# Kernel tuning notes

Hardware: AMD Instinct MI355X
Metric: run time of the kernel (lower is better)

Reference implementation:

```python
import jax, jax.numpy as jnp
import numpy as np

EMBED_DIM = 1024
NUM_HEADS = 16
HEAD_DIM = EMBED_DIM // NUM_HEADS


def setup_inputs() -> dict:
    key = jax.random.key(0)
    ks = jax.random.split(key, 11)
    B, S, D = 2, 2048, EMBED_DIM
    s = 1.0 / np.sqrt(D)
    inp = {
        "q": jax.random.normal(ks[0], (B, S, D), jnp.float32),
        "k": jax.random.normal(ks[1], (B, S, D), jnp.float32),
        "v": jax.random.normal(ks[2], (B, S, D), jnp.float32),
        # Linear params stored as (in, out) so y = x @ W + b
        "wq": jax.random.uniform(ks[3], (D, D), jnp.float32, -s, s),
        "bq": jax.random.uniform(ks[4], (D,), jnp.float32, -s, s),
        "wk": jax.random.uniform(ks[5], (D, D), jnp.float32, -s, s),
        "bk": jax.random.uniform(ks[6], (D,), jnp.float32, -s, s),
        "wv": jax.random.uniform(ks[7], (D, D), jnp.float32, -s, s),
        "bv": jax.random.uniform(ks[8], (D,), jnp.float32, -s, s),
        "wo": jax.random.uniform(ks[9], (D, D), jnp.float32, -s, s),
        "bo": jax.random.uniform(ks[10], (D,), jnp.float32, -s, s),
    }
    return inp


def reference(q, k, v, wq, bq, wk, bk, wv, bv, wo, bo):
    B, S, D = q.shape
    H, Hd = NUM_HEADS, HEAD_DIM
    temperature = Hd ** 0.5

    def proj(x, w, b):
        # (B, S, D) -> (B, H, S, Hd)
        y = x @ w + b
        return y.reshape(B, S, H, Hd).transpose(0, 2, 1, 3)

    qh = proj(q, wq, bq)
    kh = proj(k, wk, bk)
    vh = proj(v, wv, bv)

    # naive attention with materialized [B, H, S, S] scores (faithful to source)
    scores = jnp.einsum("bhqd,bhkd->bhqk", qh / temperature, kh)
    attn = jax.nn.softmax(scores, axis=-1)
    ctx = jnp.einsum("bhqk,bhkd->bhqd", attn, vh)

    ctx = ctx.transpose(0, 2, 1, 3).reshape(B, S, D)
    out = ctx @ wo + bo
    return out, attn
```

## Files before the change

### kernel.cpp

```cpp
#include <hip/hip_runtime.h>

#define S_   2048
#define D_   1024

typedef __attribute__((ext_vector_type(8))) __bf16 bf16x8;
typedef __attribute__((ext_vector_type(4))) __bf16 bf16x4;
typedef __attribute__((ext_vector_type(4))) float f32x4;
typedef __attribute__((ext_vector_type(4))) float float4v;
typedef __attribute__((ext_vector_type(2))) unsigned int u32x2;
typedef __attribute__((ext_vector_type(4))) unsigned int u32x4;

#define XQ_OFF   0
#define XK_OFF   4194304
#define XV_OFF   8388608
#define WQT_OFF  12582912
#define WKT_OFF  13631488
#define WVT_OFF  14680064
#define WOT_OFF  15728640
#define QH_OFF   16777216
#define KH_OFF   20971520
#define VHT_OFF  25165824
#define CTX_OFF  29360128
#define WS_BYTES 67108864ULL

#if __has_builtin(__builtin_amdgcn_exp2f)
#define EXP2(x) __builtin_amdgcn_exp2f(x)
#else
#define EXP2(x) __expf((x) * 0.69314718056f)
#endif
#define QSCALE 0.1803368801f

__device__ __forceinline__ unsigned short f2b(float f) {
  unsigned u = __builtin_bit_cast(unsigned, f);
  u += 0x7fffu + ((u >> 16) & 1u);
  return (unsigned short)(u >> 16);
}
__device__ __forceinline__ float b2f(unsigned s) {
  return __builtin_bit_cast(float, s << 16);
}

__global__ __launch_bounds__(256) void cvt_all(const float* __restrict__ q,
    const float* __restrict__ k, const float* __restrict__ v,
    const float* __restrict__ wq, const float* __restrict__ wk,
    const float* __restrict__ wv, const float* __restrict__ wo,
    short* __restrict__ ws) {
  __shared__ float tile[32][33];
  int b = blockIdx.x, tid = threadIdx.x;
  if (b < 12288) {
    int y = b >> 12, x = b & 4095;
    const float* src = (y == 0) ? q : (y == 1) ? k : v;
    short* dst = ws + (size_t)y * 4194304;
    size_t t = (size_t)x * 256 + tid;
    float4v f = *(const float4v*)(src + t * 4);
    u32x2 p;
    p[0] = (unsigned)f2b(f[0]) | ((unsigned)f2b(f[1]) << 16);
    p[1] = (unsigned)f2b(f[2]) | ((unsigned)f2b(f[3]) << 16);
    *(u32x2*)(dst + t * 4) = p;
    return;
  }
  int b2 = b - 12288;
  int z = b2 >> 10, rem = b2 & 1023;
  int by = rem >> 5, bx = rem & 31;
  const float* W = (z == 0) ? wq : (z == 1) ? wk : (z == 2) ? wv : wo;
  short* Wt = ws + WQT_OFF + (size_t)z * 1048576;
  int tx = tid & 31, ty = tid >> 5;
#pragma unroll
  for (int i = 0; i < 4; ++i)
    tile[ty + i * 8][tx] =
        W[(size_t)(by * 32 + ty + i * 8) * D_ + bx * 32 + tx];
  __syncthreads();
#pragma unroll
  for (int i = 0; i < 4; ++i)
    Wt[(size_t)(bx * 32 + ty + i * 8) * D_ + by * 32 + tx] =
        (short)f2b(tile[tx][ty + i * 8]);
}

__device__ __forceinline__ void stage_tile(const short* __restrict__ g,
                                           short* l, int w, int lane) {
  int lrow = lane >> 3, lcol = (lane & 7) * 8;
#pragma unroll
  for (int c = 0; c < 4; ++c) {
    int seg = c * 4 + w;
    const short* gp = g + (size_t)(seg * 8 + lrow) * 1024 + lcol;
    short* lp = l + seg * 512 + lane * 8;
    __builtin_amdgcn_global_load_lds(
        (const __attribute__((address_space(1))) void*)gp,
        (__attribute__((address_space(3))) void*)lp, 16, 0, 0);
  }
}

__global__ __launch_bounds__(256) void gemm_bf16(short* __restrict__ ws,
    const float* __restrict__ bq, const float* __restrict__ bk,
    const float* __restrict__ bv, const float* __restrict__ bo,
    float* __restrict__ out, int mode_base) {
  const int tid = threadIdx.x, lane = tid & 63, w = tid >> 6;
  const int wm = w >> 1, wn = w & 1;
  const int ln15 = lane & 15, g = lane >> 4;
  const int bm = blockIdx.y, bn = blockIdx.x;
  const int mode = (mode_base == 3) ? 3 : (int)blockIdx.z;

  const short* A; const short* Bt; const float* bias;
  if (mode == 0)      { A = ws + XQ_OFF;  Bt = ws + WQT_OFF; bias = bq; }
  else if (mode == 1) { A = ws + XK_OFF;  Bt = ws + WKT_OFF; bias = bk; }
  else if (mode == 2) { A = ws + XV_OFF;  Bt = ws + WVT_OFF; bias = bv; }
  else                { A = ws + CTX_OFF; Bt = ws + WOT_OFF; bias = bo; }

  __shared__ short smem[2][2][8192];
  short (*sA)[8192] = smem[0];
  short (*sB)[8192] = smem[1];

  f32x4 acc[4][4] = {};

  const short* Ab = A + (size_t)bm * 128 * 1024;
  const short* Bb = Bt + (size_t)bn * 128 * 1024;

  stage_tile(Ab, sA[0], w, lane);
  stage_tile(Bb, sB[0], w, lane);
  __syncthreads();

  int cur = 0;
#pragma unroll 1
  for (int kt = 0; kt < 16; ++kt) {
    if (kt < 15) {
      stage_tile(Ab + (kt + 1) * 64, sA[cur ^ 1], w, lane);
      stage_tile(Bb + (kt + 1) * 64, sB[cur ^ 1], w, lane);
    }
#pragma unroll
    for (int kk = 0; kk < 2; ++kk) {
      bf16x8 af[4], bfr[4];
#pragma unroll
      for (int m = 0; m < 4; ++m)
        af[m] = *(const bf16x8*)&sA[cur][(wm * 64 + m * 16 + ln15) * 64 + kk * 32 + g * 8];
#pragma unroll
      for (int n = 0; n < 4; ++n)
        bfr[n] = *(const bf16x8*)&sB[cur][(wn * 64 + n * 16 + ln15) * 64 + kk * 32 + g * 8];
#pragma unroll
      for (int m = 0; m < 4; ++m)
#pragma unroll
        for (int n = 0; n < 4; ++n)
          acc[m][n] = __builtin_amdgcn_mfma_f32_16x16x32_bf16(af[m], bfr[n], acc[m][n], 0, 0, 0);
    }
    __syncthreads();
    cur ^= 1;
  }

  float bb[4];
#pragma unroll
  for (int n = 0; n < 4; ++n) bb[n] = bias[bn * 128 + wn * 64 + n * 16 + ln15];

  if (mode == 3) {
#pragma unroll
    for (int m = 0; m < 4; ++m) {
      int row0 = bm * 128 + wm * 64 + m * 16 + g * 4;
#pragma unroll
      for (int n = 0; n < 4; ++n) {
        int col = bn * 128 + wn * 64 + n * 16 + ln15;
#pragma unroll
        for (int r = 0; r < 4; ++r)
          out[(size_t)(row0 + r) * 1024 + col] = acc[m][n][r] + bb[n];
      }
    }
    return;
  }

  float sc = (mode == 0) ? QSCALE : 1.0f;
  short (*tile)[136] = (short(*)[136])smem;
#pragma unroll
  for (int m = 0; m < 4; ++m)
#pragma unroll
    for (int n = 0; n < 4; ++n)
#pragma unroll
      for (int r = 0; r < 4; ++r)
        tile[wm * 64 + m * 16 + g * 4 + r][wn * 64 + n * 16 + ln15] =
            (short)f2b((acc[m][n][r] + bb[n]) * sc);
  __syncthreads();

  if (mode == 2) {
    int dcol = tid >> 1, sh = (tid & 1) * 64;
    int colg = bn * 128 + dcol, h = colg >> 6, hd = colg & 63;
    int b = bm >> 4, sblk = bm & 15;
    short* dst = ws + VHT_OFF +
                 ((size_t)((b * 16 + h) * 16 + sblk)) * 8192 + hd * 128 + sh;
#pragma unroll
    for (int j = 0; j < 8; ++j) {
      u32x4 pk;
#pragma unroll
      for (int q = 0; q < 4; ++q) {
        unsigned lo = (unsigned short)tile[sh + j * 8 + q * 2][dcol];
        unsigned hi = (unsigned short)tile[sh + j * 8 + q * 2 + 1][dcol];
        pk[q] = lo | (hi << 16);
      }
      *(u32x4*)(dst + j * 8) = pk;
    }
  } else {
    int r = tid >> 1, sh = (tid & 1) * 64;
    int colg = bn * 128 + sh, h = colg >> 6;
    int sg = bm * 128 + r, b = sg >> 11, sl = sg & 2047;
    short* dst = ws + ((mode == 0) ? QH_OFF : KH_OFF) +
                 (((size_t)(b * 16 + h)) * 2048 + sl) * 64;
#pragma unroll
    for (int j = 0; j < 8; ++j)
      *(u32x4*)(dst + j * 8) = *(const u32x4*)&tile[r][sh + j * 8];
  }
}

__global__ __launch_bounds__(512) void attn_k(short* __restrict__ ws,
                                              float* __restrict__ attn) {
  const int tid = threadIdx.x, lane = tid & 63, w = tid >> 6;
  const int ln15 = lane & 15, g = lane >> 4, ln7 = lane & 7;
  int bid = blockIdx.x;
  int qt = (bid >> 3) & 15;
  int bh = (bid & 7) + 8 * (bid >> 7);
  const int q0 = qt * 128;

  const short* Q  = ws + QH_OFF  + ((size_t)bh * 2048 + q0) * 64;
  const short* K  = ws + KH_OFF  + (size_t)bh * 2048 * 64;
  const short* Vt = ws + VHT_OFF + (size_t)bh * 131072;

  __shared__ short sKV[4][4096];
  __shared__ short PlA[128][72];
  __shared__ short PlB[128][72];

  const int srow = tid >> 3, sc = tid & 7;
  const int scsw = sc ^ (srow & 7);
  const int sdst = tid * 8;

#define STAGE1(t1, b)                                                         \
  do {                                                                        \
    __builtin_amdgcn_global_load_lds(                                         \
        (const __attribute__((address_space(1))) void*)(K + ((t1) * 128 + srow) * 64 + scsw * 8),      \
        (__attribute__((address_space(3))) void*)(&sKV[2 * (b)][sdst]), 16, 0, 0);                     \
    __builtin_amdgcn_global_load_lds(                                         \
        (const __attribute__((address_space(1))) void*)(K + ((t1) * 128 + 64 + srow) * 64 + scsw * 8), \
        (__attribute__((address_space(3))) void*)(&sKV[2 * (b) + 1][sdst]), 16, 0, 0);                 \
  } while (0)
#define STAGE_K2(kt)                                                          \
  __builtin_amdgcn_global_load_lds(                                           \
      (const __attribute__((address_space(1))) void*)(K + ((kt) * 64 + srow) * 64 + scsw * 8),         \
      (__attribute__((address_space(3))) void*)(&sKV[(kt) & 1][sdst]), 16, 0, 0)
#define STAGE_V2(kt)                                                          \
  __builtin_amdgcn_global_load_lds(                                           \
      (const __attribute__((address_space(1))) void*)(Vt + ((kt) >> 1) * 8192 + srow * 128 + ((kt) & 1) * 64 + scsw * 8), \
      (__attribute__((address_space(3))) void*)(&sKV[2 + ((kt) & 1)][sdst]), 16, 0, 0)

  bf16x8 qf0 = *(const bf16x8*)&Q[(w * 16 + ln15) * 64 + g * 8];
  bf16x8 qf1 = *(const bf16x8*)&Q[(w * 16 + ln15) * 64 + 32 + g * 8];

  STAGE1(0, 0);
  asm volatile("s_waitcnt vmcnt(0)" ::: "memory");
  __builtin_amdgcn_s_barrier();

  float ps0 = 0.f, ps1 = 0.f;
#pragma unroll 1
  for (int t = 0; t < 16; ++t) {
    int b = t & 1;
    if (t < 15) STAGE1(t + 1, b ^ 1);
#pragma unroll
    for (int m = 0; m < 8; ++m) {
      const short* kbase = &sKV[2 * b + (m >> 2)][((m * 16 + ln15) & 63) * 64];
      bf16x8 ka0 = *(const bf16x8*)&kbase[(g ^ ln7) * 8];
      bf16x8 ka1 = *(const bf16x8*)&kbase[((4 + g) ^ ln7) * 8];
      f32x4 c = {0.f, 0.f, 0.f, 0.f};
      c = __builtin_amdgcn_mfma_f32_16x16x32_bf16(ka0, qf0, c, 0, 0, 0);
      c = __builtin_amdgcn_mfma_f32_16x16x32_bf16(ka1, qf1, c, 0, 0, 0);
      ps0 += EXP2(c[0]) + EXP2(c[1]);
      ps1 += EXP2(c[2]) + EXP2(c[3]);
    }
    asm volatile("s_waitcnt vmcnt(0)" ::: "memory");
    __builtin_amdgcn_s_barrier();
  }
  float ps = ps0 + ps1;
  ps += __shfl_xor(ps, 16, 64);
  ps += __shfl_xor(ps, 32, 64);
  float ri = 1.0f / ps;

#define QKT_BODY(kti, PLW)                                                    \
  do {                                                                        \
    _Pragma("unroll") for (int m = 0; m < 4; ++m) {                           \
      const short* kbase = &sKV[(kti) & 1][(m * 16 + ln15) * 64];             \
      bf16x8 ka0 = *(const bf16x8*)&kbase[(g ^ ln7) * 8];                     \
      bf16x8 ka1 = *(const bf16x8*)&kbase[((4 + g) ^ ln7) * 8];               \
      f32x4 c = {0.f, 0.f, 0.f, 0.f};                                         \
      c = __builtin_amdgcn_mfma_f32_16x16x32_bf16(ka0, qf0, c, 0, 0, 0);      \
      c = __builtin_amdgcn_mfma_f32_16x16x32_bf16(ka1, qf1, c, 0, 0, 0);      \
      bf16x4 pb;                                                              \
      pb[0] = (__bf16)(EXP2(c[0]) * ri);                                      \
      pb[1] = (__bf16)(EXP2(c[1]) * ri);                                      \
      pb[2] = (__bf16)(EXP2(c[2]) * ri);                                      \
      pb[3] = (__bf16)(EXP2(c[3]) * ri);                                      \
      *(bf16x4*)&PLW[w * 16 + ln15][m * 16 + g * 4] = pb;                     \
    }                                                                         \
  } while (0)

#define FULL_BODY(i, PLR, PLW)                                                \
  do {                                                                        \
    if ((i) < 30) STAGE_K2((i) + 2);                                          \
    if ((i) < 31) STAGE_V2((i) + 1);                                          \
    if ((i) < 31) QKT_BODY((i) + 1, PLW);                                     \
    _Pragma("unroll") for (int kk = 0; kk < 2; ++kk) {                        \
      bf16x8 pa = *(const bf16x8*)&PLR[w * 16 + ln15][kk * 32 + g * 8];       \
      _Pragma("unroll") for (int n = 0; n < 4; ++n) {                         \
        const short* vbase = &sKV[2 + ((i) & 1)][(n * 16 + ln15) * 64];       \
        bf16x8 vb = *(const bf16x8*)&vbase[((kk * 4 + g) ^ ln7) * 8];         \
        cacc[n] = __builtin_amdgcn_mfma_f32_16x16x32_bf16(pa, vb, cacc[n], 0, 0, 0); \
      }                                                                       \
    }                                                                         \
    {                                                                         \
      float* ab = attn + ((size_t)(bh * 2048 + q0 + w * 16)) * 2048 + (i) * 64 + lane; \
      _Pragma("unroll") for (int r = 0; r < 16; ++r)                          \
        ab[(size_t)r * 2048] = b2f((unsigned short)PLR[w * 16 + r][lane]);    \
    }                                                                         \
    asm volatile("s_waitcnt vmcnt(16)" ::: "memory");                         \
    __builtin_amdgcn_s_barrier();                                             \
  } while (0)

  f32x4 cacc[4] = {};

  STAGE_K2(0);
  STAGE_V2(0);
  STAGE_K2(1);
  asm volatile("s_waitcnt vmcnt(0)" ::: "memory");
  __builtin_amdgcn_s_barrier();
  QKT_BODY(0, PlA);
  asm volatile("s_waitcnt lgkmcnt(0)" ::: "memory");
  __builtin_amdgcn_s_barrier();

#pragma unroll 1
  for (int i2 = 0; i2 < 32; i2 += 2) {
    FULL_BODY(i2, PlA, PlB);
    FULL_BODY(i2 + 1, PlB, PlA);
  }

  {
    short* Pw = &PlA[w * 16][0];
#pragma unroll
    for (int n = 0; n < 4; ++n)
#pragma unroll
      for (int r = 0; r < 4; ++r)
        Pw[(g * 4 + r) * 72 + n * 16 + ln15] = (short)f2b(cacc[n][r]);
    asm volatile("s_waitcnt lgkmcnt(0)" ::: "memory");
    __builtin_amdgcn_sched_barrier(0);
    int b = bh >> 4, h = bh & 15;
    int row = lane >> 3, col = (lane & 7) * 8;
#pragma unroll
    for (int i = 0; i < 2; ++i) {
      int q = q0 + w * 16 + i * 8 + row;
      u32x4 pk = *(const u32x4*)&Pw[(i * 8 + row) * 72 + col];
      *(u32x4*)&ws[CTX_OFF + ((size_t)(b * 2048 + q)) * 1024 + h * 64 + col] = pk;
    }
  }
#undef STAGE1
#undef STAGE_K2
#undef STAGE_V2
#undef QKT_BODY
#undef FULL_BODY
}

extern "C" void kernel_launch(void* const* d_in, const int* in_sizes, int n_in,
                              void* d_out, int out_size, void* d_ws, size_t ws_size,
                              hipStream_t stream) {
  const float* q  = (const float*)d_in[0];
  const float* k  = (const float*)d_in[1];
  const float* v  = (const float*)d_in[2];
  const float* wq = (const float*)d_in[3];
  const float* bq = (const float*)d_in[4];
  const float* wk = (const float*)d_in[5];
  const float* bk = (const float*)d_in[6];
  const float* wv = (const float*)d_in[7];
  const float* bv = (const float*)d_in[8];
  const float* wo = (const float*)d_in[9];
  const float* bo = (const float*)d_in[10];
  float* out  = (float*)d_out;
  float* attn = out + 4194304;
  short* ws = (short*)d_ws;
  if (ws_size < WS_BYTES) return;

  cvt_all<<<dim3(16384), 256, 0, stream>>>(q, k, v, wq, wk, wv, wo, ws);
  gemm_bf16<<<dim3(8, 32, 3), 256, 0, stream>>>(ws, bq, bk, bv, bo, out, 0);
  attn_k<<<dim3(512), 512, 0, stream>>>(ws, attn);
  gemm_bf16<<<dim3(8, 32, 1), 256, 0, stream>>>(ws, bq, bk, bv, bo, out, 3);
}
```

Measured before the change: 271.8 us.

## Triple-buffer K/V staging and batch attn stores into 256-column float4 writes

Restructures the attention main loop so K and V tiles use a three-deep LDS ring prefetched two steps ahead. QK^T and PV for the same tile now run back-to-back inside one iteration, replacing the previous skewed ping-pong P buffers. Probabilities for four key tiles accumulate in a wider LDS buffer and are written to the attn output as float4 stores every 256 columns, instead of scalar stores per 64 columns. This aims to improve global store efficiency and load latency hiding. The cost is more LDS, which may reduce occupancy, and an added lgkmcnt wait between QK and PV within each step.

```diff
diff --git a/kernel.cpp b/kernel.cpp
--- a/kernel.cpp
+++ b/kernel.cpp
@@ -217,31 +217,30 @@
   const short* K  = ws + KH_OFF  + (size_t)bh * 2048 * 64;
   const short* Vt = ws + VHT_OFF + (size_t)bh * 131072;
 
-  __shared__ short sKV[4][4096];
-  __shared__ short PlA[128][72];
-  __shared__ short PlB[128][72];
+  __shared__ short sStage[6][4096];
+  __shared__ short Pbig[128][264];
 
   const int srow = tid >> 3, sc = tid & 7;
   const int scsw = sc ^ (srow & 7);
   const int sdst = tid * 8;
 
+#define STAGE_K2(kt)                                                          \
+  __builtin_amdgcn_global_load_lds(                                           \
+      (const __attribute__((address_space(1))) void*)(K + ((kt) * 64 + srow) * 64 + scsw * 8),         \
+      (__attribute__((address_space(3))) void*)(&sStage[(kt) % 3][sdst]), 16, 0, 0)
+#define STAGE_V2(kt)                                                          \
+  __builtin_amdgcn_global_load_lds(                                           \
+      (const __attribute__((address_space(1))) void*)(Vt + ((kt) >> 1) * 8192 + srow * 128 + ((kt) & 1) * 64 + scsw * 8), \
+      (__attribute__((address_space(3))) void*)(&sStage[3 + (kt) % 3][sdst]), 16, 0, 0)
 #define STAGE1(t1, b)                                                         \
   do {                                                                        \
     __builtin_amdgcn_global_load_lds(                                         \
         (const __attribute__((address_space(1))) void*)(K + ((t1) * 128 + srow) * 64 + scsw * 8),      \
-        (__attribute__((address_space(3))) void*)(&sKV[2 * (b)][sdst]), 16, 0, 0);                     \
+        (__attribute__((address_space(3))) void*)(&sStage[(b)][sdst]), 16, 0, 0);                      \
     __builtin_amdgcn_global_load_lds(                                         \
         (const __attribute__((address_space(1))) void*)(K + ((t1) * 128 + 64 + srow) * 64 + scsw * 8), \
-        (__attribute__((address_space(3))) void*)(&sKV[2 * (b) + 1][sdst]), 16, 0, 0);                 \
+        (__attribute__((address_space(3))) void*)(&sStage[3 + (b)][sdst]), 16, 0, 0);                  \
   } while (0)
-#define STAGE_K2(kt)                                                          \
-  __builtin_amdgcn_global_load_lds(                                           \
-      (const __attribute__((address_space(1))) void*)(K + ((kt) * 64 + srow) * 64 + scsw * 8),         \
-      (__attribute__((address_space(3))) void*)(&sKV[(kt) & 1][sdst]), 16, 0, 0)
-#define STAGE_V2(kt)                                                          \
-  __builtin_amdgcn_global_load_lds(                                           \
-      (const __attribute__((address_space(1))) void*)(Vt + ((kt) >> 1) * 8192 + srow * 128 + ((kt) & 1) * 64 + scsw * 8), \
-      (__attribute__((address_space(3))) void*)(&sKV[2 + ((kt) & 1)][sdst]), 16, 0, 0)
 
   bf16x8 qf0 = *(const bf16x8*)&Q[(w * 16 + ln15) * 64 + g * 8];
   bf16x8 qf1 = *(const bf16x8*)&Q[(w * 16 + ln15) * 64 + 32 + g * 8];
@@ -257,7 +256,8 @@
     if (t < 15) STAGE1(t + 1, b ^ 1);
 #pragma unroll
     for (int m = 0; m < 8; ++m) {
-      const short* kbase = &sKV[2 * b + (m >> 2)][((m * 16 + ln15) & 63) * 64];
+      const short* kbase =
+          &sStage[(m >> 2) * 3 + b][((m * 16 + ln15) & 63) * 64];
       bf16x8 ka0 = *(const bf16x8*)&kbase[(g ^ ln7) * 8];
       bf16x8 ka1 = *(const bf16x8*)&kbase[((4 + g) ^ ln7) * 8];
       f32x4 c = {0.f, 0.f, 0.f, 0.f};
@@ -274,70 +274,87 @@
   ps += __shfl_xor(ps, 32, 64);
   float ri = 1.0f / ps;
 
-#define QKT_BODY(kti, PLW)                                                    \
-  do {                                                                        \
-    _Pragma("unroll") for (int m = 0; m < 4; ++m) {                           \
-      const short* kbase = &sKV[(kti) & 1][(m * 16 + ln15) * 64];             \
-      bf16x8 ka0 = *(const bf16x8*)&kbase[(g ^ ln7) * 8];                     \
-      bf16x8 ka1 = *(const bf16x8*)&kbase[((4 + g) ^ ln7) * 8];               \
-      f32x4 c = {0.f, 0.f, 0.f, 0.f};                                         \
-      c = __builtin_amdgcn_mfma_f32_16x16x32_bf16(ka0, qf0, c, 0, 0, 0);      \
-      c = __builtin_amdgcn_mfma_f32_16x16x32_bf16(ka1, qf1, c, 0, 0, 0);      \
-      bf16x4 pb;                                                              \
-      pb[0] = (__bf16)(EXP2(c[0]) * ri);                                      \
-      pb[1] = (__bf16)(EXP2(c[1]) * ri);                                      \
-      pb[2] = (__bf16)(EXP2(c[2]) * ri);                                      \
-      pb[3] = (__bf16)(EXP2(c[3]) * ri);                                      \
-      *(bf16x4*)&PLW[w * 16 + ln15][m * 16 + g * 4] = pb;                     \
-    }                                                                         \
-  } while (0)
-
-#define FULL_BODY(i, PLR, PLW)                                                \
-  do {                                                                        \
-    if ((i) < 30) STAGE_K2((i) + 2);                                          \
-    if ((i) < 31) STAGE_V2((i) + 1);                                          \
-    if ((i) < 31) QKT_BODY((i) + 1, PLW);                                     \
-    _Pragma("unroll") for (int kk = 0; kk < 2; ++kk) {                        \
-      bf16x8 pa = *(const bf16x8*)&PLR[w * 16 + ln15][kk * 32 + g * 8];       \
-      _Pragma("unroll") for (int n = 0; n < 4; ++n) {                         \
-        const short* vbase = &sKV[2 + ((i) & 1)][(n * 16 + ln15) * 64];       \
-        bf16x8 vb = *(const bf16x8*)&vbase[((kk * 4 + g) ^ ln7) * 8];         \
-        cacc[n] = __builtin_amdgcn_mfma_f32_16x16x32_bf16(pa, vb, cacc[n], 0, 0, 0); \
-      }                                                                       \
-    }                                                                         \
-    {                                                                         \
-      float* ab = attn + ((size_t)(bh * 2048 + q0 + w * 16)) * 2048 + (i) * 64 + lane; \
-      _Pragma("unroll") for (int r = 0; r < 16; ++r)                          \
-        ab[(size_t)r * 2048] = b2f((unsigned short)PLR[w * 16 + r][lane]);    \
-    }                                                                         \
-    asm volatile("s_waitcnt vmcnt(16)" ::: "memory");                         \
-    __builtin_amdgcn_s_barrier();                                             \
-  } while (0)
-
   f32x4 cacc[4] = {};
 
   STAGE_K2(0);
   STAGE_V2(0);
   STAGE_K2(1);
-  asm volatile("s_waitcnt vmcnt(0)" ::: "memory");
+  STAGE_V2(1);
+  asm volatile("s_waitcnt vmcnt(2)" ::: "memory");
   __builtin_amdgcn_s_barrier();
-  QKT_BODY(0, PlA);
-  asm volatile("s_waitcnt lgkmcnt(0)" ::: "memory");
-  __builtin_amdgcn_s_barrier();
 
 #pragma unroll 1
-  for (int i2 = 0; i2 < 32; i2 += 2) {
-    FULL_BODY(i2, PlA, PlB);
-    FULL_BODY(i2 + 1, PlB, PlA);
+  for (int s = 0; s < 8; ++s) {
+#pragma unroll
+    for (int j = 0; j < 4; ++j) {
+      const int kt = s * 4 + j;
+      const int ktm3 = kt % 3;
+      if (kt < 30) {
+        STAGE_K2(kt + 2);
+        STAGE_V2(kt + 2);
+      }
+#pragma unroll
+      for (int m = 0; m < 4; ++m) {
+        const short* kbase = &sStage[ktm3][(m * 16 + ln15) * 64];
+        bf16x8 ka0 = *(const bf16x8*)&kbase[(g ^ ln7) * 8];
+        bf16x8 ka1 = *(const bf16x8*)&kbase[((4 + g) ^ ln7) * 8];
+        f32x4 c = {0.f, 0.f, 0.f, 0.f};
+        c = __builtin_amdgcn_mfma_f32_16x16x32_bf16(ka0, qf0, c, 0, 0, 0);
+        c = __builtin_amdgcn_mfma_f32_16x16x32_bf16(ka1, qf1, c, 0, 0, 0);
+        bf16x4 pb;
+        pb[0] = (__bf16)(EXP2(c[0]) * ri);
+        pb[1] = (__bf16)(EXP2(c[1]) * ri);
+        pb[2] = (__bf16)(EXP2(c[2]) * ri);
+        pb[3] = (__bf16)(EXP2(c[3]) * ri);
+        *(bf16x4*)&Pbig[w * 16 + ln15][j * 64 + m * 16 + g * 4] = pb;
+      }
+      asm volatile("s_waitcnt lgkmcnt(0)" ::: "memory");
+      __builtin_amdgcn_sched_barrier(0);
+
+#pragma unroll
+      for (int kk = 0; kk < 2; ++kk) {
+        bf16x8 pa =
+            *(const bf16x8*)&Pbig[w * 16 + ln15][j * 64 + kk * 32 + g * 8];
+#pragma unroll
+        for (int n = 0; n < 4; ++n) {
+          const short* vbase = &sStage[3 + ktm3][(n * 16 + ln15) * 64];
+          bf16x8 vb = *(const bf16x8*)&vbase[((kk * 4 + g) ^ ln7) * 8];
+          cacc[n] =
+              __builtin_amdgcn_mfma_f32_16x16x32_bf16(pa, vb, cacc[n], 0, 0, 0);
+        }
+      }
+
+      if (kt >= 30) {
+        asm volatile("s_waitcnt vmcnt(0)" ::: "memory");
+      } else if (j == 0 && s > 0) {
+        asm volatile("s_waitcnt vmcnt(18)" ::: "memory");
+      } else {
+        asm volatile("s_waitcnt vmcnt(2)" ::: "memory");
+      }
+      __builtin_amdgcn_s_barrier();
+    }
+
+    float* ab = attn + ((size_t)(bh * 2048 + q0 + w * 16)) * 2048 + s * 256 +
+                lane * 4;
+#pragma unroll
+    for (int r = 0; r < 16; ++r) {
+      u32x2 pv = *(const u32x2*)&Pbig[w * 16 + r][lane * 4];
+      float4v o;
+      o[0] = b2f(pv[0] & 0xffffu);
+      o[1] = b2f(pv[0] >> 16);
+      o[2] = b2f(pv[1] & 0xffffu);
+      o[3] = b2f(pv[1] >> 16);
+      *(float4v*)(ab + (size_t)r * 2048) = o;
+    }
   }
 
   {
-    short* Pw = &PlA[w * 16][0];
+    short* Pw = &Pbig[w * 16][0];
 #pragma unroll
     for (int n = 0; n < 4; ++n)
 #pragma unroll
       for (int r = 0; r < 4; ++r)
-        Pw[(g * 4 + r) * 72 + n * 16 + ln15] = (short)f2b(cacc[n][r]);
+        Pw[(g * 4 + r) * 264 + n * 16 + ln15] = (short)f2b(cacc[n][r]);
     asm volatile("s_waitcnt lgkmcnt(0)" ::: "memory");
     __builtin_amdgcn_sched_barrier(0);
     int b = bh >> 4, h = bh & 15;
@@ -345,15 +362,13 @@
 #pragma unroll
     for (int i = 0; i < 2; ++i) {
       int q = q0 + w * 16 + i * 8 + row;
-      u32x4 pk = *(const u32x4*)&Pw[(i * 8 + row) * 72 + col];
+      u32x4 pk = *(const u32x4*)&Pw[(i * 8 + row) * 264 + col];
       *(u32x4*)&ws[CTX_OFF + ((size_t)(b * 2048 + q)) * 1024 + h * 64 + col] = pk;
     }
   }
-#undef STAGE1
 #undef STAGE_K2
 #undef STAGE_V2
-#undef QKT_BODY
-#undef FULL_BODY
+#undef STAGE1
 }
 
 extern "C" void kernel_launch(void* const* d_in, const int* in_sizes, int n_in,
```

New measurement: 294.9 us. 1.08x slower.
